# Kernel optimization log

Measured on AMD Instinct MI355X. Metric: run time of the kernel, lower is better.

The kernel has to match this reference:

```python
import jax, jax.numpy as jnp
import numpy as np

LEVELS = 16
FEATURES = 2
HASHMAP_SIZE = 524288
BASE_RES = 16
PER_LEVEL_SCALE = 1.3819

_P1, _P2, _P3 = np.uint32(73856093), np.uint32(19349663), np.uint32(83492791)
# 8 trilinear corner offsets, bit order (x, y, z)
_OFFSETS = np.array([[ox, oy, oz] for ox in (0, 1) for oy in (0, 1) for oz in (0, 1)], dtype=np.int32)


def setup_inputs() -> dict:
    key = jax.random.key(0)
    kx, kt = jax.random.split(key)
    x = jax.random.uniform(kx, (2000000, 3), dtype=jnp.float32)
    tables = jax.random.normal(kt, (LEVELS, HASHMAP_SIZE, FEATURES), dtype=jnp.float32) * 0.01
    return {"x": x, "tables": tables}


def _hash_coords(corners_u32):
    # corners_u32: [N, 8, 3] uint32; spatial hash with uint32 wraparound.
    h = (corners_u32[..., 0] * _P1) ^ (corners_u32[..., 1] * _P2) ^ (corners_u32[..., 2] * _P3)
    return (h % np.uint32(HASHMAP_SIZE)).astype(jnp.int32)  # [N, 8]


def _encode(x, tables):
    offsets_i = jnp.asarray(_OFFSETS)                 # [8, 3] int32
    offsets_f = offsets_i.astype(x.dtype)             # [8, 3]
    embeds = []
    for l in range(LEVELS):
        res = int(BASE_RES * PER_LEVEL_SCALE ** l)
        pos = x * res                                  # [N, 3]
        pos_floor = jnp.floor(pos)
        w = pos - pos_floor                            # [N, 3] trilinear weights
        base = pos_floor.astype(jnp.int32)             # non-negative (x in [0,1])
        corners = (base[:, None, :] + offsets_i).astype(jnp.uint32)  # [N, 8, 3]
        idx = _hash_coords(corners)                    # [N, 8]
        vals = tables[l][idx]                          # [N, 8, F] gather
        # weight per corner = prod over axes of (w if offset else 1-w)
        wgt = jnp.prod(offsets_f * w[:, None, :] + (1.0 - offsets_f) * (1.0 - w[:, None, :]), axis=-1)  # [N, 8]
        embeds.append(jnp.einsum('nc,ncf->nf', wgt, vals))  # [N, F]
    return jnp.concatenate(embeds, axis=-1)           # [N, LEVELS*F]


def reference(x, tables):
    return _encode(x, tables)
```

## Files before the change

### kernel.cpp

```cpp
#include <hip/hip_runtime.h>
#include <hip/hip_fp16.h>
#include <stdint.h>

#define LEVELS 16
#define FEAT 2
#define TABLE_SIZE 524288
#define TMASK (TABLE_SIZE - 1)

typedef float f32x2 __attribute__((ext_vector_type(2)));
typedef float f32x4 __attribute__((ext_vector_type(4)));
typedef float f32x4u __attribute__((ext_vector_type(4), aligned(8)));

__device__ __constant__ int kRes[LEVELS] = {
    16, 22, 30, 42, 58, 80, 111, 153, 212, 294, 406, 561, 775, 1072, 1481, 2047
};

#define P1 73856093u
#define P2 19349663u
#define P3 83492791u

#define NQLEV 8
#define HASH0 8
#define NHASH (LEVELS - HASH0)

constexpr int   cQD[NQLEV]     = { 17, 23, 31, 43, 59, 81, 112, 154 };
constexpr float cQRes[NQLEV]   = { 16.0f, 22.0f, 30.0f, 42.0f, 58.0f, 80.0f, 111.0f, 153.0f };
constexpr int   cQCum[NQLEV+1] = { 0, 4913, 17080, 46871, 126378, 331757, 863198, 2268126, 5920390 };
#define NCELLS 5920390

__global__ __launch_bounds__(256) void remap1_kernel(
    const float* __restrict__ tables,
    f32x2* __restrict__ dense)
{
    const int d = blockIdx.x * 256 + threadIdx.x;
    if (d >= NCELLS) return;
    int l = 0;
#pragma unroll
    for (int k = 1; k < NQLEV; ++k)
        if (d >= cQCum[k]) l = k;
    const int D   = cQD[l];
    const int rel = d - cQCum[l];
    const uint32_t bx = rel / (D * D);
    const uint32_t r  = rel - bx * (D * D);
    const uint32_t by = r / D;
    const uint32_t bz = r - by * D;
    const uint32_t slot = ((bx * P1) ^ (by * P2) ^ (bz * P3)) & TMASK;
    const f32x2* __restrict__ tab = reinterpret_cast<const f32x2*>(tables) + (size_t)l * TABLE_SIZE;
    dense[d] = tab[slot];
}

__global__ __launch_bounds__(256) void remap2_kernel(
    const f32x2* __restrict__ dense,
    uint4* __restrict__ qtab)
{
    const int d = blockIdx.x * 256 + threadIdx.x;
    if (d >= NCELLS) return;
    int l = 0;
#pragma unroll
    for (int k = 1; k < NQLEV; ++k)
        if (d >= cQCum[k]) l = k;
    const int D   = cQD[l];
    const int rel = d - cQCum[l];

    const f32x2* __restrict__ dl = dense + cQCum[l];
    const f32x4u a = *reinterpret_cast<const f32x4u*>(dl + rel);
    const f32x4u b = *reinterpret_cast<const f32x4u*>(dl + rel + D);

    union { __half2 h; uint32_t u; } p0, p1, p2, p3;
    p0.h = __float22half2_rn(make_float2(a.x, a.y));
    p1.h = __float22half2_rn(make_float2(a.z, a.w));
    p2.h = __float22half2_rn(make_float2(b.x, b.y));
    p3.h = __float22half2_rn(make_float2(b.z, b.w));
    qtab[d] = make_uint4(p0.u, p1.u, p2.u, p3.u);
}

__global__ __launch_bounds__(256) void encode_level_kernel(
    const float* __restrict__ x,
    const float* __restrict__ tables,
    f32x2* __restrict__ ws,
    int n, int nb, int l0)
{
    const int l   = l0 + blockIdx.x / nb;
    const int blk = blockIdx.x - (l - l0) * nb;
    const int t   = threadIdx.x;
    const int p0  = blk * 512;

    __shared__ float sx[512 * 3];
    const long long total3 = (long long)n * 3;
    const long long gbase  = (long long)p0 * 3;
#pragma unroll
    for (int k = 0; k < 6; ++k) {
        long long g = gbase + k * 256 + t;
        sx[k * 256 + t] = (g < total3) ? __builtin_nontemporal_load(x + g) : 0.0f;
    }
    __syncthreads();

    const float resf = (float)kRes[l];
    const f32x2* __restrict__ tab = reinterpret_cast<const f32x2*>(tables) + (size_t)l * TABLE_SIZE;

    uint32_t idx[2][8];
    float    wgt[2][8];
#pragma unroll
    for (int s = 0; s < 2; ++s) {
        const int tp = s * 256 + t;
        const float fx = sx[3 * tp + 0] * resf;
        const float fy = sx[3 * tp + 1] * resf;
        const float fz = sx[3 * tp + 2] * resf;
        const float flx = floorf(fx), fly = floorf(fy), flz = floorf(fz);
        const float wx = fx - flx, wy = fy - fly, wz = fz - flz;
        const float ux = 1.0f - wx, uy = 1.0f - wy, uz = 1.0f - wz;
        const uint32_t hx0 = (uint32_t)(int)flx * P1, hx1 = hx0 + P1;
        const uint32_t hy0 = (uint32_t)(int)fly * P2, hy1 = hy0 + P2;
        const uint32_t hz0 = (uint32_t)(int)flz * P3, hz1 = hz0 + P3;
#pragma unroll
        for (int c = 0; c < 8; ++c) {
            const uint32_t hx = (c & 4) ? hx1 : hx0;
            const uint32_t hy = (c & 2) ? hy1 : hy0;
            const uint32_t hz = (c & 1) ? hz1 : hz0;
            idx[s][c] = (hx ^ hy ^ hz) & TMASK;
            wgt[s][c] = ((c & 4) ? wx : ux) * ((c & 2) ? wy : uy) * ((c & 1) ? wz : uz);
        }
    }

    f32x2 v[2][8];
#pragma unroll
    for (int s = 0; s < 2; ++s)
#pragma unroll
        for (int c = 0; c < 8; ++c)
            v[s][c] = tab[idx[s][c]];

#pragma unroll
    for (int s = 0; s < 2; ++s) {
        float f0 = 0.0f, f1 = 0.0f;
#pragma unroll
        for (int c = 0; c < 8; ++c) {
            f0 = fmaf(wgt[s][c], v[s][c].x, f0);
            f1 = fmaf(wgt[s][c], v[s][c].y, f1);
        }
        const int i = p0 + s * 256 + t;
        if (i < n) {
            f32x2 r; r.x = f0; r.y = f1;
            __builtin_nontemporal_store(r, ws + (size_t)(l - l0) * n + i);
        }
    }
}

__global__ __launch_bounds__(256) void finalize_kernel(
    const float* __restrict__ x,
    const uint4* __restrict__ qtab,
    const f32x2* __restrict__ ws,
    float* __restrict__ out,
    int n)
{
    __shared__ float s[256 * 33];
    __shared__ float sx[256 * 3];
    const int t  = threadIdx.x;
    const int p0 = blockIdx.x * 256;
    const int m  = min(256, n - p0);

    const long long total3 = (long long)n * 3;
    const long long gbase  = (long long)p0 * 3;
#pragma unroll
    for (int k = 0; k < 3; ++k) {
        long long g = gbase + k * 256 + t;
        sx[k * 256 + t] = (g < total3) ? __builtin_nontemporal_load(x + g) : 0.0f;
    }
    __syncthreads();

    if (t < m) {
        const int i = p0 + t;

        f32x2 h[NHASH];
#pragma unroll
        for (int j = 0; j < NHASH; ++j)
            h[j] = __builtin_nontemporal_load(ws + (size_t)j * n + i);

        const float px = sx[3 * t + 0];
        const float py = sx[3 * t + 1];
        const float pz = sx[3 * t + 2];

#pragma unroll
        for (int l = 0; l < NQLEV; ++l) {
            const int   D    = cQD[l];
            const int   DD   = D * D;
            const float resf = cQRes[l];
            const uint4* __restrict__ qt = qtab + cQCum[l];

            const float fx = px * resf, fy = py * resf, fz = pz * resf;
            const float flx = floorf(fx), fly = floorf(fy), flz = floorf(fz);
            const float wx = fx - flx, wy = fy - fly, wz = fz - flz;
            const float ux = 1.0f - wx, uy = 1.0f - wy, uz = 1.0f - wz;
            const int q0 = (((int)flx * D + (int)fly) * D + (int)flz);

            const uint4 A = qt[q0];
            const uint4 B = qt[q0 + DD];

            union { uint32_t u; __half2 hh; } c;
            float2 a00, a01, a10, a11, b00, b01, b10, b11;
            c.u = A.x; a00 = __half22float2(c.hh);
            c.u = A.y; a01 = __half22float2(c.hh);
            c.u = A.z; a10 = __half22float2(c.hh);
            c.u = A.w; a11 = __half22float2(c.hh);
            c.u = B.x; b00 = __half22float2(c.hh);
            c.u = B.y; b01 = __half22float2(c.hh);
            c.u = B.z; b10 = __half22float2(c.hh);
            c.u = B.w; b11 = __half22float2(c.hh);

            const float ya0 = fmaf(uz, a00.x, wz * a01.x), ya1 = fmaf(uz, a10.x, wz * a11.x);
            const float yb0 = fmaf(uz, b00.x, wz * b01.x), yb1 = fmaf(uz, b10.x, wz * b11.x);
            const float f0  = fmaf(ux, fmaf(uy, ya0, wy * ya1), wx * fmaf(uy, yb0, wy * yb1));
            const float za0 = fmaf(uz, a00.y, wz * a01.y), za1 = fmaf(uz, a10.y, wz * a11.y);
            const float zb0 = fmaf(uz, b00.y, wz * b01.y), zb1 = fmaf(uz, b10.y, wz * b11.y);
            const float f1  = fmaf(ux, fmaf(uy, za0, wy * za1), wx * fmaf(uy, zb0, wy * zb1));

            s[t * 33 + 2 * l + 0] = f0;
            s[t * 33 + 2 * l + 1] = f1;
        }
#pragma unroll
        for (int j = 0; j < NHASH; ++j) {
            s[t * 33 + 2 * (NQLEV + j) + 0] = h[j].x;
            s[t * 33 + 2 * (NQLEV + j) + 1] = h[j].y;
        }
    }
    __syncthreads();

    const int nchunk = m * 8;
    f32x4* __restrict__ o4 = reinterpret_cast<f32x4*>(out) + (size_t)p0 * 8;
#pragma unroll
    for (int j = 0; j < 8; ++j) {
        const int cl = j * 256 + t;
        if (cl < nchunk) {
            const int p = cl >> 3, ch = cl & 7;
            f32x4 q;
            q.x = s[p * 33 + ch * 4 + 0];
            q.y = s[p * 33 + ch * 4 + 1];
            q.z = s[p * 33 + ch * 4 + 2];
            q.w = s[p * 33 + ch * 4 + 3];
            __builtin_nontemporal_store(q, o4 + cl);
        }
    }
}

__global__ __launch_bounds__(256) void hashgrid_enc_kernel(
    const float* __restrict__ x,
    const float* __restrict__ tables,
    float* __restrict__ out,
    int n)
{
    __shared__ float sx[256 * 3];
    const int t = threadIdx.x;
    const int block0 = blockIdx.x * 256;
    const long long total3 = (long long)n * 3;
    const long long gbase = (long long)block0 * 3;
#pragma unroll
    for (int k = 0; k < 3; ++k) {
        long long g = gbase + k * 256 + t;
        sx[k * 256 + t] = (g < total3) ? x[g] : 0.0f;
    }
    __syncthreads();
    const int i = block0 + t;
    if (i >= n) return;
    const float px = sx[3 * t + 0];
    const float py = sx[3 * t + 1];
    const float pz = sx[3 * t + 2];
    float outv[2 * LEVELS];
#pragma unroll
    for (int l = 0; l < LEVELS; ++l) {
        const float resf = (float)kRes[l];
        const float fx = px * resf, fy = py * resf, fz = pz * resf;
        const float flx = floorf(fx), fly = floorf(fy), flz = floorf(fz);
        const float wx = fx - flx, wy = fy - fly, wz = fz - flz;
        const float ux = 1.0f - wx, uy = 1.0f - wy, uz = 1.0f - wz;
        const uint32_t hx0 = (uint32_t)(int)flx * P1, hx1 = hx0 + P1;
        const uint32_t hy0 = (uint32_t)(int)fly * P2, hy1 = hy0 + P2;
        const uint32_t hz0 = (uint32_t)(int)flz * P3, hz1 = hz0 + P3;
        const float* __restrict__ tab = tables + (size_t)l * (TABLE_SIZE * FEAT);
        float f0 = 0.0f, f1 = 0.0f;
#pragma unroll
        for (int c = 0; c < 8; ++c) {
            const uint32_t hx = (c & 4) ? hx1 : hx0;
            const uint32_t hy = (c & 2) ? hy1 : hy0;
            const uint32_t hz = (c & 1) ? hz1 : hz0;
            const uint32_t idx = (hx ^ hy ^ hz) & TMASK;
            const float2 v = *reinterpret_cast<const float2*>(tab + (size_t)idx * FEAT);
            const float w = ((c & 4) ? wx : ux) * ((c & 2) ? wy : uy) * ((c & 1) ? wz : uz);
            f0 = fmaf(w, v.x, f0);
            f1 = fmaf(w, v.y, f1);
        }
        outv[2 * l + 0] = f0;
        outv[2 * l + 1] = f1;
    }
    float4* __restrict__ o4 = reinterpret_cast<float4*>(out + (size_t)i * (2 * LEVELS));
#pragma unroll
    for (int k = 0; k < 8; ++k) {
        o4[k] = make_float4(outv[4 * k + 0], outv[4 * k + 1],
                            outv[4 * k + 2], outv[4 * k + 3]);
    }
}

extern "C" void kernel_launch(void* const* d_in, const int* in_sizes, int n_in,
                              void* d_out, int out_size, void* d_ws, size_t ws_size,
                              hipStream_t stream) {
    const float* x = (const float*)d_in[0];
    const float* tables = (const float*)d_in[1];
    float* out = (float*)d_out;
    const int n = in_sizes[0] / 3;

    const size_t stag_b = (size_t)NHASH * (size_t)n * sizeof(f32x2);
    const size_t s1_b   = ((size_t)NCELLS + 256) * sizeof(f32x2);
    const size_t r0_b   = (stag_b > s1_b ? stag_b : s1_b);
    const size_t qoff   = (r0_b + 15) & ~(size_t)15;
    const size_t need   = qoff + (size_t)NCELLS * sizeof(uint4);

    if (ws_size >= need) {
        f32x2* staging = (f32x2*)d_ws;
        f32x2* stage1  = (f32x2*)d_ws;
        uint4* qtab    = (uint4*)((char*)d_ws + qoff);

        const int nbcell = (NCELLS + 255) / 256;
        hipLaunchKernelGGL(remap1_kernel, dim3(nbcell), dim3(256), 0, stream, tables, stage1);
        hipLaunchKernelGGL(remap2_kernel, dim3(nbcell), dim3(256), 0, stream, stage1, qtab);

        const int nb512 = (n + 511) / 512;
        hipLaunchKernelGGL(encode_level_kernel, dim3(nb512 * NHASH), dim3(256), 0, stream,
                           x, tables, staging, n, nb512, HASH0);

        const int nb256 = (n + 255) / 256;
        hipLaunchKernelGGL(finalize_kernel, dim3(nb256), dim3(256), 0, stream,
                           x, qtab, staging, out, n);
    } else {
        const int nb = (n + 255) / 256;
        hipLaunchKernelGGL(hashgrid_enc_kernel, dim3(nb), dim3(256), 0, stream,
                           x, tables, out, n);
    }
}
```

Baseline: 1.020 ms.

## Move level 7 to hash path and split dense levels 5-6 into separate kernel

Level 7 no longer uses the remapped dense fp16 corner table and falls back to the per-level hash gather kernel. This shrinks the dense remap from about 5.9M cells to about 2.3M, which cuts remap cost and workspace. Dense levels 5 and 6 are moved out of finalize into a new per-level kernel that writes to staging, so finalize only computes levels 0-4 inline and reads 11 staged levels. The goal is a smaller per-level cache working set and less remap work, at the cost of an extra launch and more staging traffic.

```diff
diff --git a/kernel.cpp b/kernel.cpp
--- a/kernel.cpp
+++ b/kernel.cpp
@@ -19,14 +19,16 @@
 #define P2 19349663u
 #define P3 83492791u
 
-#define NQLEV 8
-#define HASH0 8
+#define NQ 7
+#define HASH0 7
 #define NHASH (LEVELS - HASH0)
-
-constexpr int   cQD[NQLEV]     = { 17, 23, 31, 43, 59, 81, 112, 154 };
-constexpr float cQRes[NQLEV]   = { 16.0f, 22.0f, 30.0f, 42.0f, 58.0f, 80.0f, 111.0f, 153.0f };
-constexpr int   cQCum[NQLEV+1] = { 0, 4913, 17080, 46871, 126378, 331757, 863198, 2268126, 5920390 };
-#define NCELLS 5920390
+#define NSTAGE (LEVELS - 5)
+#define NFIN 5
+
+constexpr int   cQD[NQ]     = { 17, 23, 31, 43, 59, 81, 112 };
+constexpr float cQRes[NQ]   = { 16.0f, 22.0f, 30.0f, 42.0f, 58.0f, 80.0f, 111.0f };
+constexpr int   cQCum[NQ+1] = { 0, 4913, 17080, 46871, 126378, 331757, 863198, 2268126 };
+#define NCELLS 2268126
 
 __global__ __launch_bounds__(256) void remap1_kernel(
     const float* __restrict__ tables,
@@ -36,7 +38,7 @@
     if (d >= NCELLS) return;
     int l = 0;
 #pragma unroll
-    for (int k = 1; k < NQLEV; ++k)
+    for (int k = 1; k < NQ; ++k)
         if (d >= cQCum[k]) l = k;
     const int D   = cQD[l];
     const int rel = d - cQCum[l];
@@ -57,7 +59,7 @@
     if (d >= NCELLS) return;
     int l = 0;
 #pragma unroll
-    for (int k = 1; k < NQLEV; ++k)
+    for (int k = 1; k < NQ; ++k)
         if (d >= cQCum[k]) l = k;
     const int D   = cQD[l];
     const int rel = d - cQCum[l];
@@ -140,7 +142,84 @@
         const int i = p0 + s * 256 + t;
         if (i < n) {
             f32x2 r; r.x = f0; r.y = f1;
-            __builtin_nontemporal_store(r, ws + (size_t)(l - l0) * n + i);
+            __builtin_nontemporal_store(r, ws + (size_t)(l - 5) * n + i);
+        }
+    }
+}
+
+__global__ __launch_bounds__(256) void encode_dense56_kernel(
+    const float* __restrict__ x,
+    const uint4* __restrict__ qtab,
+    f32x2* __restrict__ ws,
+    int n, int nb)
+{
+    const int lsel = blockIdx.x / nb;
+    const int blk  = blockIdx.x - lsel * nb;
+    const int t    = threadIdx.x;
+    const int p0   = blk * 512;
+
+    __shared__ float sx[512 * 3];
+    const long long total3 = (long long)n * 3;
+    const long long gbase  = (long long)p0 * 3;
+#pragma unroll
+    for (int k = 0; k < 6; ++k) {
+        long long g = gbase + k * 256 + t;
+        sx[k * 256 + t] = (g < total3) ? __builtin_nontemporal_load(x + g) : 0.0f;
+    }
+    __syncthreads();
+
+    const int   D    = lsel ? 112 : 81;
+    const int   DD   = D * D;
+    const float resf = lsel ? 111.0f : 80.0f;
+    const uint4* __restrict__ qt = qtab + (lsel ? cQCum[6] : cQCum[5]);
+
+    int   q0a[2];
+    float wxa[2], wya[2], wza[2];
+#pragma unroll
+    for (int s = 0; s < 2; ++s) {
+        const int tp = s * 256 + t;
+        const float fx = sx[3 * tp + 0] * resf;
+        const float fy = sx[3 * tp + 1] * resf;
+        const float fz = sx[3 * tp + 2] * resf;
+        const float flx = floorf(fx), fly = floorf(fy), flz = floorf(fz);
+        wxa[s] = fx - flx; wya[s] = fy - fly; wza[s] = fz - flz;
+        q0a[s] = ((int)flx * D + (int)fly) * D + (int)flz;
+    }
+
+    uint4 A[2], B[2];
+#pragma unroll
+    for (int s = 0; s < 2; ++s) {
+        A[s] = qt[q0a[s]];
+        B[s] = qt[q0a[s] + DD];
+    }
+
+#pragma unroll
+    for (int s = 0; s < 2; ++s) {
+        const float wx = wxa[s], wy = wya[s], wz = wza[s];
+        const float ux = 1.0f - wx, uy = 1.0f - wy, uz = 1.0f - wz;
+
+        union { uint32_t u; __half2 hh; } c;
+        float2 a00, a01, a10, a11, b00, b01, b10, b11;
+        c.u = A[s].x; a00 = __half22float2(c.hh);
+        c.u = A[s].y; a01 = __half22float2(c.hh);
+        c.u = A[s].z; a10 = __half22float2(c.hh);
+        c.u = A[s].w; a11 = __half22float2(c.hh);
+        c.u = B[s].x; b00 = __half22float2(c.hh);
+        c.u = B[s].y; b01 = __half22float2(c.hh);
+        c.u = B[s].z; b10 = __half22float2(c.hh);
+        c.u = B[s].w; b11 = __half22float2(c.hh);
+
+        const float ya0 = fmaf(uz, a00.x, wz * a01.x), ya1 = fmaf(uz, a10.x, wz * a11.x);
+        const float yb0 = fmaf(uz, b00.x, wz * b01.x), yb1 = fmaf(uz, b10.x, wz * b11.x);
+        const float f0  = fmaf(ux, fmaf(uy, ya0, wy * ya1), wx * fmaf(uy, yb0, wy * yb1));
+        const float za0 = fmaf(uz, a00.y, wz * a01.y), za1 = fmaf(uz, a10.y, wz * a11.y);
+        const float zb0 = fmaf(uz, b00.y, wz * b01.y), zb1 = fmaf(uz, b10.y, wz * b11.y);
+        const float f1  = fmaf(ux, fmaf(uy, za0, wy * za1), wx * fmaf(uy, zb0, wy * zb1));
+
+        const int i = p0 + s * 256 + t;
+        if (i < n) {
+            f32x2 r; r.x = f0; r.y = f1;
+            __builtin_nontemporal_store(r, ws + (size_t)lsel * n + i);
         }
     }
 }
@@ -170,9 +249,9 @@
     if (t < m) {
         const int i = p0 + t;
 
-        f32x2 h[NHASH];
-#pragma unroll
-        for (int j = 0; j < NHASH; ++j)
+        f32x2 h[NSTAGE];
+#pragma unroll
+        for (int j = 0; j < NSTAGE; ++j)
             h[j] = __builtin_nontemporal_load(ws + (size_t)j * n + i);
 
         const float px = sx[3 * t + 0];
@@ -180,7 +259,7 @@
         const float pz = sx[3 * t + 2];
 
 #pragma unroll
-        for (int l = 0; l < NQLEV; ++l) {
+        for (int l = 0; l < NFIN; ++l) {
             const int   D    = cQD[l];
             const int   DD   = D * D;
             const float resf = cQRes[l];
@@ -217,9 +296,9 @@
             s[t * 33 + 2 * l + 1] = f1;
         }
 #pragma unroll
-        for (int j = 0; j < NHASH; ++j) {
-            s[t * 33 + 2 * (NQLEV + j) + 0] = h[j].x;
-            s[t * 33 + 2 * (NQLEV + j) + 1] = h[j].y;
+        for (int j = 0; j < NSTAGE; ++j) {
+            s[t * 33 + 2 * (NFIN + j) + 0] = h[j].x;
+            s[t * 33 + 2 * (NFIN + j) + 1] = h[j].y;
         }
     }
     __syncthreads();
@@ -306,7 +385,7 @@
     float* out = (float*)d_out;
     const int n = in_sizes[0] / 3;
 
-    const size_t stag_b = (size_t)NHASH * (size_t)n * sizeof(f32x2);
+    const size_t stag_b = (size_t)NSTAGE * (size_t)n * sizeof(f32x2);
     const size_t s1_b   = ((size_t)NCELLS + 256) * sizeof(f32x2);
     const size_t r0_b   = (stag_b > s1_b ? stag_b : s1_b);
     const size_t qoff   = (r0_b + 15) & ~(size_t)15;
@@ -324,6 +403,8 @@
         const int nb512 = (n + 511) / 512;
         hipLaunchKernelGGL(encode_level_kernel, dim3(nb512 * NHASH), dim3(256), 0, stream,
                            x, tables, staging, n, nb512, HASH0);
+        hipLaunchKernelGGL(encode_dense56_kernel, dim3(nb512 * 2), dim3(256), 0, stream,
+                           x, qtab, staging, n, nb512);
 
         const int nb256 = (n + 255) / 256;
         hipLaunchKernelGGL(finalize_kernel, dim3(nb256), dim3(256), 0, stream,
```

Result: faster. 970.9 us (-4.9%).
